# Performance work log

Hardware: AMD Instinct MI355X
Metric: run time of the kernel (lower is better)

## Reference

```python
import jax, jax.numpy as jnp
import numpy as np

N_NODES = 50000
N_EDGES = 800000
IN_FEATS = 96
HIDDEN = 48


def setup_inputs() -> dict:
    key = jax.random.key(0)
    ks = jax.random.split(key, 16)
    x = jax.random.normal(ks[0], (N_NODES, IN_FEATS), dtype=jnp.float32)
    edge_index = jax.random.randint(ks[1], (2, N_EDGES), 0, N_NODES, dtype=jnp.int32)

    def lin(k, fan_in, fan_out):
        s = 1.0 / np.sqrt(fan_in)
        return jax.random.uniform(k, (fan_in, fan_out), jnp.float32, -s, s)

    return {
        "x": x,
        "edge_index": edge_index,
        # SAGEConv layer 0: in -> hidden
        "w_self0": lin(ks[2], IN_FEATS, HIDDEN),
        "w_neigh0": lin(ks[3], IN_FEATS, HIDDEN),
        "b0": jnp.zeros((HIDDEN,), jnp.float32),
        # SAGEConv layer 1: hidden -> hidden
        "w_self1": lin(ks[4], HIDDEN, HIDDEN),
        "w_neigh1": lin(ks[5], HIDDEN, HIDDEN),
        "b1": jnp.zeros((HIDDEN,), jnp.float32),
        # SAGEConv layer 2: hidden -> hidden
        "w_self2": lin(ks[6], HIDDEN, HIDDEN),
        "w_neigh2": lin(ks[7], HIDDEN, HIDDEN),
        "b2": jnp.zeros((HIDDEN,), jnp.float32),
        # prediction head: hidden -> 1
        "w_pred": lin(ks[8], HIDDEN, 1),
        "b_pred": jnp.zeros((1,), jnp.float32),
    }


def _sage_mean(x, src, dst, deg_inv, w_self, w_neigh, b):
    # mean over in-neighbors: gather src features, segment-sum at dst, / in-degree
    agg = jax.ops.segment_sum(x[src], dst, num_segments=N_NODES) * deg_inv  # [N, F]
    return x @ w_self + agg @ w_neigh + b


def reference(x, edge_index, w_self0, w_neigh0, b0, w_self1, w_neigh1, b1,
              w_self2, w_neigh2, b2, w_pred, b_pred):
    src, dst = edge_index[0], edge_index[1]
    deg = jax.ops.segment_sum(jnp.ones((src.shape[0],), x.dtype), dst,
                              num_segments=N_NODES)
    deg_inv = (1.0 / jnp.maximum(deg, 1.0))[:, None]  # isolated nodes -> 0 agg

    h = jax.nn.relu(_sage_mean(x, src, dst, deg_inv, w_self0, w_neigh0, b0))
    h = jax.nn.relu(_sage_mean(h, src, dst, deg_inv, w_self1, w_neigh1, b1))
    h = jax.nn.relu(_sage_mean(h, src, dst, deg_inv, w_self2, w_neigh2, b2))
    return h @ w_pred + b_pred  # [N, 1]
```

## Files before the change

kernel.cpp:

```cpp
#include <hip/hip_runtime.h>
#include <hip/hip_fp16.h>


constexpr int HID = 48;
constexpr int MAXDEG = 64;
constexpr int GNB = 64;

__device__ __forceinline__ unsigned pack_h2(float a, float b) {
    __half2 h = __floats2half2_rn(a, b);
    return *reinterpret_cast<unsigned*>(&h);
}
__device__ __forceinline__ void acc_u2(float* g, uint2 u) {
    __half2 h0 = *reinterpret_cast<__half2*>(&u.x);
    __half2 h1 = *reinterpret_cast<__half2*>(&u.y);
    float2 f0 = __half22float2(h0), f1 = __half22float2(h1);
    g[0] += f0.x; g[1] += f0.y; g[2] += f1.x; g[3] += f1.y;
}
__device__ __forceinline__ void unpack_u2(float* v, uint2 u) {
    __half2 h0 = *reinterpret_cast<__half2*>(&u.x);
    __half2 h1 = *reinterpret_cast<__half2*>(&u.y);
    float2 f0 = __half22float2(h0), f1 = __half22float2(h1);
    v[0] = f0.x; v[1] = f0.y; v[2] = f1.x; v[3] = f1.y;
}
__device__ __forceinline__ void fma12_h(const uint2* __restrict__ wrow, float s,
                                        float* acc) {
    uint2 w0 = wrow[0], w1 = wrow[1], w2 = wrow[2];
    float v[12];
    unpack_u2(v + 0, w0); unpack_u2(v + 4, w1); unpack_u2(v + 8, w2);
#pragma unroll
    for (int j = 0; j < 12; ++j) acc[j] = fmaf(s, v[j], acc[j]);
}

__device__ __forceinline__ void gather_h8(const __half* __restrict__ p,
                                          const unsigned short* __restrict__ bkt,
                                          uint4 pv0, uint4 pv1, int deg, int e,
                                          int jb, int zrow, float* g) {
    float ga[12], gb[12];
#pragma unroll
    for (int j = 0; j < 12; ++j) { ga[j] = 0.0f; gb[j] = 0.0f; }
    const int sh = 16 * e;
    int idx[8];
    {
        unsigned w[8] = {pv0.x, pv0.y, pv0.z, pv0.w, pv1.x, pv1.y, pv1.z, pv1.w};
#pragma unroll
        for (int r = 0; r < 8; ++r) {
            int k = 2 * r + e;
            idx[r] = (k < deg) ? (int)((w[r] >> sh) & 0xffffu) : zrow;
        }
    }
    {
        const uint2* r0 = reinterpret_cast<const uint2*>(p + (size_t)idx[0] * HID + jb);
        const uint2* r1 = reinterpret_cast<const uint2*>(p + (size_t)idx[1] * HID + jb);
        const uint2* r2 = reinterpret_cast<const uint2*>(p + (size_t)idx[2] * HID + jb);
        const uint2* r3 = reinterpret_cast<const uint2*>(p + (size_t)idx[3] * HID + jb);
        uint2 a0 = r0[0], a1 = r0[1], a2 = r0[2];
        uint2 b0 = r1[0], b1 = r1[1], b2 = r1[2];
        uint2 c0 = r2[0], c1 = r2[1], c2 = r2[2];
        uint2 d0 = r3[0], d1 = r3[1], d2 = r3[2];
        acc_u2(ga + 0, a0); acc_u2(ga + 4, a1); acc_u2(ga + 8, a2);
        acc_u2(gb + 0, b0); acc_u2(gb + 4, b1); acc_u2(gb + 8, b2);
        acc_u2(ga + 0, c0); acc_u2(ga + 4, c1); acc_u2(ga + 8, c2);
        acc_u2(gb + 0, d0); acc_u2(gb + 4, d1); acc_u2(gb + 8, d2);
    }
    {
        const uint2* r0 = reinterpret_cast<const uint2*>(p + (size_t)idx[4] * HID + jb);
        const uint2* r1 = reinterpret_cast<const uint2*>(p + (size_t)idx[5] * HID + jb);
        const uint2* r2 = reinterpret_cast<const uint2*>(p + (size_t)idx[6] * HID + jb);
        const uint2* r3 = reinterpret_cast<const uint2*>(p + (size_t)idx[7] * HID + jb);
        uint2 a0 = r0[0], a1 = r0[1], a2 = r0[2];
        uint2 b0 = r1[0], b1 = r1[1], b2 = r1[2];
        uint2 c0 = r2[0], c1 = r2[1], c2 = r2[2];
        uint2 d0 = r3[0], d1 = r3[1], d2 = r3[2];
        acc_u2(ga + 0, a0); acc_u2(ga + 4, a1); acc_u2(ga + 8, a2);
        acc_u2(gb + 0, b0); acc_u2(gb + 4, b1); acc_u2(gb + 8, b2);
        acc_u2(ga + 0, c0); acc_u2(ga + 4, c1); acc_u2(ga + 8, c2);
        acc_u2(gb + 0, d0); acc_u2(gb + 4, d1); acc_u2(gb + 8, d2);
    }
    int i = 16 + e;
    for (; i + 6 < deg; i += 8) {
        int s0 = bkt[i], s1 = bkt[i + 2], s2 = bkt[i + 4], s3 = bkt[i + 6];
        const uint2* r0 = reinterpret_cast<const uint2*>(p + (size_t)s0 * HID + jb);
        const uint2* r1 = reinterpret_cast<const uint2*>(p + (size_t)s1 * HID + jb);
        const uint2* r2 = reinterpret_cast<const uint2*>(p + (size_t)s2 * HID + jb);
        const uint2* r3 = reinterpret_cast<const uint2*>(p + (size_t)s3 * HID + jb);
        uint2 a0 = r0[0], a1 = r0[1], a2 = r0[2];
        uint2 b0 = r1[0], b1 = r1[1], b2 = r1[2];
        uint2 c0 = r2[0], c1 = r2[1], c2 = r2[2];
        uint2 d0 = r3[0], d1 = r3[1], d2 = r3[2];
        acc_u2(ga + 0, a0); acc_u2(ga + 4, a1); acc_u2(ga + 8, a2);
        acc_u2(gb + 0, b0); acc_u2(gb + 4, b1); acc_u2(gb + 8, b2);
        acc_u2(ga + 0, c0); acc_u2(ga + 4, c1); acc_u2(ga + 8, c2);
        acc_u2(gb + 0, d0); acc_u2(gb + 4, d1); acc_u2(gb + 8, d2);
    }
    for (; i + 2 < deg; i += 4) {
        int s0 = bkt[i], s1 = bkt[i + 2];
        const uint2* r0 = reinterpret_cast<const uint2*>(p + (size_t)s0 * HID + jb);
        const uint2* r1 = reinterpret_cast<const uint2*>(p + (size_t)s1 * HID + jb);
        uint2 a0 = r0[0], a1 = r0[1], a2 = r0[2];
        uint2 b0 = r1[0], b1 = r1[1], b2 = r1[2];
        acc_u2(ga + 0, a0); acc_u2(ga + 4, a1); acc_u2(ga + 8, a2);
        acc_u2(gb + 0, b0); acc_u2(gb + 4, b1); acc_u2(gb + 8, b2);
    }
    if (i < deg) {
        const uint2* r0 = reinterpret_cast<const uint2*>(p + (size_t)bkt[i] * HID + jb);
        uint2 a0 = r0[0], a1 = r0[1], a2 = r0[2];
        acc_u2(ga + 0, a0); acc_u2(ga + 4, a1); acc_u2(ga + 8, a2);
    }
#pragma unroll
    for (int j = 0; j < 12; ++j) g[j] = ga[j] + gb[j];
#pragma unroll
    for (int j = 0; j < 12; ++j) g[j] += __shfl_xor(g[j], 4, 64);
}

__global__ __launch_bounds__(128) void fill_proj_k(
    const float* __restrict__ X, const float* __restrict__ Wn,
    const float* __restrict__ Ws, const float* __restrict__ bias,
    __half* __restrict__ p_out, float* __restrict__ s_out, int n_nodes,
    const int* __restrict__ src, const int* __restrict__ dst,
    int* __restrict__ cnt, unsigned short* __restrict__ buckets,
    int n_edges, int gemm_blocks, int cstride) {
    __shared__ float wlds[96 * HID];
    __shared__ float bias_lds[HID];
    const int t = threadIdx.x;

    if ((int)blockIdx.x >= gemm_blocks) {
        int base = (blockIdx.x - gemm_blocks) * 512 + t;
#pragma unroll
        for (int u = 0; u < 4; ++u) {
            int eidx = base + u * 128;
            if (eidx < n_edges) {
                int d = dst[eidx];
                int s = src[eidx];
                int pos = atomicAdd(&cnt[(size_t)d * cstride], 1);
                if (pos < MAXDEG) buckets[(size_t)d * MAXDEG + pos] = (unsigned short)s;
            }
        }
        return;
    }

    if (blockIdx.x == 0 && t < 24)
        reinterpret_cast<unsigned*>(p_out + (size_t)n_nodes * HID)[t] = 0u;

    const int q = t & 3;
    const int m = t >> 2;
    const int jb = q * 12;
    const int n0 = blockIdx.x * GNB + 2 * m;
    const int n1 = n0 + 1;
    const bool v0 = n0 < n_nodes, v1 = n1 < n_nodes;
    const int cn0 = v0 ? n0 : 0, cn1 = v1 ? n1 : 0;
    const float4* xr0 = reinterpret_cast<const float4*>(X + (size_t)cn0 * 96);
    const float4* xr1 = reinterpret_cast<const float4*>(X + (size_t)cn1 * 96);

    for (int i = t; i < 96 * HID; i += 128) wlds[i] = Wn[i];
    __syncthreads();
    {
        float pa[12], pb[12];
#pragma unroll
        for (int j = 0; j < 12; ++j) { pa[j] = 0.0f; pb[j] = 0.0f; }
#pragma unroll 4
        for (int k4 = 0; k4 < 24; ++k4) {
            float4 xa = xr0[k4];
            float4 xb = xr1[k4];
#pragma unroll
            for (int c = 0; c < 4; ++c) {
                float x0 = (c == 0) ? xa.x : (c == 1) ? xa.y : (c == 2) ? xa.z : xa.w;
                float x1 = (c == 0) ? xb.x : (c == 1) ? xb.y : (c == 2) ? xb.z : xb.w;
                const float4* wr =
                    reinterpret_cast<const float4*>(&wlds[(k4 * 4 + c) * HID + jb]);
#pragma unroll
                for (int j4 = 0; j4 < 3; ++j4) {
                    float4 wv = wr[j4];
                    pa[j4 * 4 + 0] = fmaf(x0, wv.x, pa[j4 * 4 + 0]);
                    pa[j4 * 4 + 1] = fmaf(x0, wv.y, pa[j4 * 4 + 1]);
                    pa[j4 * 4 + 2] = fmaf(x0, wv.z, pa[j4 * 4 + 2]);
                    pa[j4 * 4 + 3] = fmaf(x0, wv.w, pa[j4 * 4 + 3]);
                    pb[j4 * 4 + 0] = fmaf(x1, wv.x, pb[j4 * 4 + 0]);
                    pb[j4 * 4 + 1] = fmaf(x1, wv.y, pb[j4 * 4 + 1]);
                    pb[j4 * 4 + 2] = fmaf(x1, wv.z, pb[j4 * 4 + 2]);
                    pb[j4 * 4 + 3] = fmaf(x1, wv.w, pb[j4 * 4 + 3]);
                }
            }
        }
        if (v0) {
            uint2* po = reinterpret_cast<uint2*>(p_out + (size_t)n0 * HID + jb);
            po[0] = make_uint2(pack_h2(pa[0], pa[1]), pack_h2(pa[2], pa[3]));
            po[1] = make_uint2(pack_h2(pa[4], pa[5]), pack_h2(pa[6], pa[7]));
            po[2] = make_uint2(pack_h2(pa[8], pa[9]), pack_h2(pa[10], pa[11]));
        }
        if (v1) {
            uint2* po = reinterpret_cast<uint2*>(p_out + (size_t)n1 * HID + jb);
            po[0] = make_uint2(pack_h2(pb[0], pb[1]), pack_h2(pb[2], pb[3]));
            po[1] = make_uint2(pack_h2(pb[4], pb[5]), pack_h2(pb[6], pb[7]));
            po[2] = make_uint2(pack_h2(pb[8], pb[9]), pack_h2(pb[10], pb[11]));
        }
    }
    __syncthreads();

    for (int i = t; i < 96 * HID; i += 128) wlds[i] = Ws[i];
    if (t < HID) bias_lds[t] = bias[t];
    __syncthreads();
    {
        float sa[12], sb[12];
#pragma unroll
        for (int j = 0; j < 12; ++j) {
            float b = bias_lds[jb + j];
            sa[j] = b; sb[j] = b;
        }
#pragma unroll 4
        for (int k4 = 0; k4 < 24; ++k4) {
            float4 xa = xr0[k4];
            float4 xb = xr1[k4];
#pragma unroll
            for (int c = 0; c < 4; ++c) {
                float x0 = (c == 0) ? xa.x : (c == 1) ? xa.y : (c == 2) ? xa.z : xa.w;
                float x1 = (c == 0) ? xb.x : (c == 1) ? xb.y : (c == 2) ? xb.z : xb.w;
                const float4* wr =
                    reinterpret_cast<const float4*>(&wlds[(k4 * 4 + c) * HID + jb]);
#pragma unroll
                for (int j4 = 0; j4 < 3; ++j4) {
                    float4 wv = wr[j4];
                    sa[j4 * 4 + 0] = fmaf(x0, wv.x, sa[j4 * 4 + 0]);
                    sa[j4 * 4 + 1] = fmaf(x0, wv.y, sa[j4 * 4 + 1]);
                    sa[j4 * 4 + 2] = fmaf(x0, wv.z, sa[j4 * 4 + 2]);
                    sa[j4 * 4 + 3] = fmaf(x0, wv.w, sa[j4 * 4 + 3]);
                    sb[j4 * 4 + 0] = fmaf(x1, wv.x, sb[j4 * 4 + 0]);
                    sb[j4 * 4 + 1] = fmaf(x1, wv.y, sb[j4 * 4 + 1]);
                    sb[j4 * 4 + 2] = fmaf(x1, wv.z, sb[j4 * 4 + 2]);
                    sb[j4 * 4 + 3] = fmaf(x1, wv.w, sb[j4 * 4 + 3]);
                }
            }
        }
        float4* so0 = reinterpret_cast<float4*>(s_out + (size_t)cn0 * HID + jb);
        float4* so1 = reinterpret_cast<float4*>(s_out + (size_t)cn1 * HID + jb);
#pragma unroll
        for (int j4 = 0; j4 < 3; ++j4) {
            if (v0) so0[j4] = make_float4(sa[j4 * 4 + 0], sa[j4 * 4 + 1],
                                          sa[j4 * 4 + 2], sa[j4 * 4 + 3]);
            if (v1) so1[j4] = make_float4(sb[j4 * 4 + 0], sb[j4 * 4 + 1],
                                          sb[j4 * 4 + 2], sb[j4 * 4 + 3]);
        }
    }
}

__global__ __launch_bounds__(128, 6) void act_k(
    const __half* __restrict__ p_in, const float* __restrict__ s_in,
    const int* __restrict__ cnt, const unsigned short* __restrict__ buckets,
    __half* __restrict__ h_out, int n_nodes, int cstride) {
    const int t = threadIdx.x;
    if (blockIdx.x == 0 && t < 24)
        reinterpret_cast<unsigned*>(h_out + (size_t)n_nodes * HID)[t] = 0u;
    const int q = t & 3;
    const int e = (t >> 2) & 1;
    const int m = t >> 3;
    const int n = blockIdx.x * 16 + m;
    if (n >= n_nodes) return;
    const int jb = q * 12;

    const int deg_raw = cnt[(size_t)n * cstride];
    const unsigned short* bkt = buckets + (size_t)n * MAXDEG;
    const uint4 pv0 = reinterpret_cast<const uint4*>(bkt)[0];
    const uint4 pv1 = reinterpret_cast<const uint4*>(bkt)[1];
    float4 sv0, sv1, sv2;
    if (e == 0) {
        const float4* sr = reinterpret_cast<const float4*>(s_in + (size_t)n * HID + jb);
        sv0 = sr[0]; sv1 = sr[1]; sv2 = sr[2];
    }

    const int deg = min(deg_raw, MAXDEG);
    const float di = 1.0f / fmaxf((float)deg, 1.0f);
    float g[12];
    gather_h8(p_in, bkt, pv0, pv1, deg, e, jb, n_nodes, g);

    if (e == 0) {
        float h[12];
        h[0] = fmaxf(fmaf(di, g[0], sv0.x), 0.0f);
        h[1] = fmaxf(fmaf(di, g[1], sv0.y), 0.0f);
        h[2] = fmaxf(fmaf(di, g[2], sv0.z), 0.0f);
        h[3] = fmaxf(fmaf(di, g[3], sv0.w), 0.0f);
        h[4] = fmaxf(fmaf(di, g[4], sv1.x), 0.0f);
        h[5] = fmaxf(fmaf(di, g[5], sv1.y), 0.0f);
        h[6] = fmaxf(fmaf(di, g[6], sv1.z), 0.0f);
        h[7] = fmaxf(fmaf(di, g[7], sv1.w), 0.0f);
        h[8] = fmaxf(fmaf(di, g[8], sv2.x), 0.0f);
        h[9] = fmaxf(fmaf(di, g[9], sv2.y), 0.0f);
        h[10] = fmaxf(fmaf(di, g[10], sv2.z), 0.0f);
        h[11] = fmaxf(fmaf(di, g[11], sv2.w), 0.0f);
        uint2* ho = reinterpret_cast<uint2*>(h_out + (size_t)n * HID + jb);
        ho[0] = make_uint2(pack_h2(h[0], h[1]), pack_h2(h[2], h[3]));
        ho[1] = make_uint2(pack_h2(h[4], h[5]), pack_h2(h[6], h[7]));
        ho[2] = make_uint2(pack_h2(h[8], h[9]), pack_h2(h[10], h[11]));
    }
}

template <bool LAST>
__global__ __launch_bounds__(128, 6) void layer_k(
    const __half* __restrict__ h_in, const int* __restrict__ cnt,
    const unsigned short* __restrict__ buckets, const float* __restrict__ wn,
    const float* __restrict__ ws, const float* __restrict__ bn,
    const float* __restrict__ w_pred, const float* __restrict__ b_pred,
    __half* __restrict__ h_out, float* __restrict__ out, int n_nodes,
    int cstride) {
    __shared__ uint2 wn_s[HID * HID / 4];
    __shared__ uint2 ws_s[HID * HID / 4];
    __shared__ float bn_lds[HID];
    __shared__ float wp_lds[HID];

    const int t = threadIdx.x;
    const int q = t & 3;
    const int e = (t >> 2) & 1;
    const int m = t >> 3;
    const int n = blockIdx.x * 16 + m;
    const bool nv = n < n_nodes;
    const int cn = nv ? n : 0;
    const int jb = q * 12;

    if (!LAST && blockIdx.x == 0 && t < 24)
        reinterpret_cast<unsigned*>(h_out + (size_t)n_nodes * HID)[t] = 0u;

    const int deg_raw = cnt[(size_t)cn * cstride];
    const unsigned short* bkt = buckets + (size_t)cn * MAXDEG;
    const uint4 pv0 = reinterpret_cast<const uint4*>(bkt)[0];
    const uint4 pv1 = reinterpret_cast<const uint4*>(bkt)[1];
    const uint2* hr = reinterpret_cast<const uint2*>(h_in + (size_t)cn * HID + jb);
    uint2 ha = hr[0], hb = hr[1], hc = hr[2];

    for (int i4 = t; i4 < HID * HID / 4; i4 += 128) {
        float4 a = reinterpret_cast<const float4*>(wn)[i4];
        float4 b = reinterpret_cast<const float4*>(ws)[i4];
        wn_s[i4] = make_uint2(pack_h2(a.x, a.y), pack_h2(a.z, a.w));
        ws_s[i4] = make_uint2(pack_h2(b.x, b.y), pack_h2(b.z, b.w));
    }
    if (t < HID) bn_lds[t] = bn[t];
    if (LAST && t < HID) wp_lds[t] = w_pred[t];
    __syncthreads();

    if (!nv) return;

    const int deg = min(deg_raw, MAXDEG);
    const float di = 1.0f / fmaxf((float)deg, 1.0f);
    float g[12];
    gather_h8(h_in, bkt, pv0, pv1, deg, e, jb, n_nodes, g);
#pragma unroll
    for (int j = 0; j < 12; ++j) g[j] *= di;

    float hs_own[12];
    unpack_u2(hs_own + 0, ha); unpack_u2(hs_own + 4, hb); unpack_u2(hs_own + 8, hc);

    float acc[12];
#pragma unroll
    for (int j = 0; j < 12; ++j) acc[j] = (e == 0) ? bn_lds[jb + j] : 0.0f;

    const int kb = e * 24;
#pragma unroll
    for (int kk = 0; kk < 24; ++kk) {
        const int k = kb + kk;
        const int srcl = (t & ~3) | (k / 12);
        float gs = __shfl(g[kk % 12], srcl, 64);
        float hv = __shfl(hs_own[kk % 12], srcl, 64);
        fma12_h(&wn_s[(k * HID + jb) >> 2], gs, acc);
        fma12_h(&ws_s[(k * HID + jb) >> 2], hv, acc);
    }
#pragma unroll
    for (int j = 0; j < 12; ++j) acc[j] += __shfl_xor(acc[j], 4, 64);

    if (LAST) {
        float s = 0.0f;
#pragma unroll
        for (int j = 0; j < 12; ++j) s = fmaf(fmaxf(acc[j], 0.0f), wp_lds[jb + j], s);
        s += __shfl_xor(s, 1, 64);
        s += __shfl_xor(s, 2, 64);
        if ((t & 7) == 0) out[n] = s + b_pred[0];
        return;
    }

    if (e == 0) {
        float h[12];
#pragma unroll
        for (int j = 0; j < 12; ++j) h[j] = fmaxf(acc[j], 0.0f);
        uint2* ho = reinterpret_cast<uint2*>(h_out + (size_t)n * HID + jb);
        ho[0] = make_uint2(pack_h2(h[0], h[1]), pack_h2(h[2], h[3]));
        ho[1] = make_uint2(pack_h2(h[4], h[5]), pack_h2(h[6], h[7]));
        ho[2] = make_uint2(pack_h2(h[8], h[9]), pack_h2(h[10], h[11]));
    }
}

extern "C" void kernel_launch(void* const* d_in, const int* in_sizes, int n_in,
                              void* d_out, int out_size, void* d_ws, size_t ws_size,
                              hipStream_t stream) {
    const float* x        = (const float*)d_in[0];
    const int*   ei       = (const int*)d_in[1];
    const float* w_self0  = (const float*)d_in[2];
    const float* w_neigh0 = (const float*)d_in[3];
    const float* b0       = (const float*)d_in[4];
    const float* w_self1  = (const float*)d_in[5];
    const float* w_neigh1 = (const float*)d_in[6];
    const float* b1       = (const float*)d_in[7];
    const float* w_self2  = (const float*)d_in[8];
    const float* w_neigh2 = (const float*)d_in[9];
    const float* b2       = (const float*)d_in[10];
    const float* w_pred   = (const float*)d_in[11];
    const float* b_pred   = (const float*)d_in[12];

    const int n_nodes = in_sizes[0] / 96;
    const int n_edges = in_sizes[1] / 2;
    const int* src = ei;
    const int* dst = ei + n_edges;

    const size_t need_fixed = (size_t)n_nodes * MAXDEG * 2
                            + 3 * ((size_t)(n_nodes + 1) * HID * 2)
                            + (size_t)n_nodes * HID * 4;
    int cstride = (need_fixed + (size_t)n_nodes * 4 * 4 <= ws_size) ? 4 : 1;

    char* wsb = (char*)d_ws;
    int* cnt                = (int*)wsb;              wsb += (size_t)n_nodes * cstride * 4;
    unsigned short* buckets = (unsigned short*)wsb;   wsb += (size_t)n_nodes * MAXDEG * 2;
    __half* p0 = (__half*)wsb;                        wsb += (size_t)(n_nodes + 1) * HID * 2;
    __half* h1 = (__half*)wsb;                        wsb += (size_t)(n_nodes + 1) * HID * 2;
    __half* h2 = (__half*)wsb;                        wsb += (size_t)(n_nodes + 1) * HID * 2;
    float* s0 = (float*)wsb;                          wsb += (size_t)n_nodes * HID * 4;
    float* out = (float*)d_out;

    const int gnb = (n_nodes + GNB - 1) / GNB;
    const int fb = (n_edges + 511) / 512;
    const int lb = (n_nodes + 15) / 16;

    hipMemsetAsync(cnt, 0, (size_t)n_nodes * cstride * 4, stream);

    fill_proj_k<<<gnb + fb, 128, 0, stream>>>(x, w_neigh0, w_self0, b0, p0, s0,
                                              n_nodes, src, dst, cnt, buckets,
                                              n_edges, gnb, cstride);
    act_k<<<lb, 128, 0, stream>>>(p0, s0, cnt, buckets, h1, n_nodes, cstride);
    layer_k<false><<<lb, 128, 0, stream>>>(h1, cnt, buckets, w_neigh1, w_self1,
                                           b1, nullptr, nullptr, h2, nullptr,
                                           n_nodes, cstride);
    layer_k<true><<<lb, 128, 0, stream>>>(h2, cnt, buckets, w_neigh2, w_self2,
                                          b2, w_pred, b_pred, nullptr, out,
                                          n_nodes, cstride);
}
```

Baseline: 216.6 us.

## Move layer-0 self projection into aggregation kernel and pad feature rows to 64

The self-term projection x@W_self0+b0 moves out of the fill/projection kernel and into act_k, which recomputes it from x while doing the neighbor gather. This removes the fp32 s0 intermediate write and read. Feature rows are padded to a 64-half stride so each row sits on one 128-byte line, and the gather is templated to prefetch 4 or 2 index vectors up front. In exchange act_k holds an 18KB weight tile in LDS and its occupancy hint drops to 4, and it rereads x.

```diff
diff --git a/kernel.cpp b/kernel.cpp
--- a/kernel.cpp
+++ b/kernel.cpp
@@ -4,6 +4,7 @@
 
 constexpr int HID = 48;
 constexpr int MAXDEG = 64;
+constexpr int RSTRIDE = 64;
 constexpr int GNB = 64;
 
 __device__ __forceinline__ unsigned pack_h2(float a, float b) {
@@ -31,28 +32,26 @@
     for (int j = 0; j < 12; ++j) acc[j] = fmaf(s, v[j], acc[j]);
 }
 
-__device__ __forceinline__ void gather_h8(const __half* __restrict__ p,
-                                          const unsigned short* __restrict__ bkt,
-                                          uint4 pv0, uint4 pv1, int deg, int e,
-                                          int jb, int zrow, float* g) {
+template <int NB>
+__device__ __forceinline__ void gather_pad(const __half* __restrict__ p,
+                                           const unsigned short* __restrict__ bkt,
+                                           const uint4 (&pw)[NB], int deg, int e,
+                                           int jb, int zrow, float* g) {
     float ga[12], gb[12];
 #pragma unroll
     for (int j = 0; j < 12; ++j) { ga[j] = 0.0f; gb[j] = 0.0f; }
     const int sh = 16 * e;
-    int idx[8];
-    {
-        unsigned w[8] = {pv0.x, pv0.y, pv0.z, pv0.w, pv1.x, pv1.y, pv1.z, pv1.w};
-#pragma unroll
-        for (int r = 0; r < 8; ++r) {
-            int k = 2 * r + e;
-            idx[r] = (k < deg) ? (int)((w[r] >> sh) & 0xffffu) : zrow;
-        }
-    }
-    {
-        const uint2* r0 = reinterpret_cast<const uint2*>(p + (size_t)idx[0] * HID + jb);
-        const uint2* r1 = reinterpret_cast<const uint2*>(p + (size_t)idx[1] * HID + jb);
-        const uint2* r2 = reinterpret_cast<const uint2*>(p + (size_t)idx[2] * HID + jb);
-        const uint2* r3 = reinterpret_cast<const uint2*>(p + (size_t)idx[3] * HID + jb);
+#pragma unroll
+    for (int b = 0; b < NB; ++b) {
+        const int k0 = 8 * b + e;
+        int i0 = (k0 < deg)     ? (int)((pw[b].x >> sh) & 0xffffu) : zrow;
+        int i1 = (k0 + 2 < deg) ? (int)((pw[b].y >> sh) & 0xffffu) : zrow;
+        int i2 = (k0 + 4 < deg) ? (int)((pw[b].z >> sh) & 0xffffu) : zrow;
+        int i3 = (k0 + 6 < deg) ? (int)((pw[b].w >> sh) & 0xffffu) : zrow;
+        const uint2* r0 = reinterpret_cast<const uint2*>(p + (size_t)i0 * RSTRIDE + jb);
+        const uint2* r1 = reinterpret_cast<const uint2*>(p + (size_t)i1 * RSTRIDE + jb);
+        const uint2* r2 = reinterpret_cast<const uint2*>(p + (size_t)i2 * RSTRIDE + jb);
+        const uint2* r3 = reinterpret_cast<const uint2*>(p + (size_t)i3 * RSTRIDE + jb);
         uint2 a0 = r0[0], a1 = r0[1], a2 = r0[2];
         uint2 b0 = r1[0], b1 = r1[1], b2 = r1[2];
         uint2 c0 = r2[0], c1 = r2[1], c2 = r2[2];
@@ -62,11 +61,13 @@
         acc_u2(ga + 0, c0); acc_u2(ga + 4, c1); acc_u2(ga + 8, c2);
         acc_u2(gb + 0, d0); acc_u2(gb + 4, d1); acc_u2(gb + 8, d2);
     }
-    {
-        const uint2* r0 = reinterpret_cast<const uint2*>(p + (size_t)idx[4] * HID + jb);
-        const uint2* r1 = reinterpret_cast<const uint2*>(p + (size_t)idx[5] * HID + jb);
-        const uint2* r2 = reinterpret_cast<const uint2*>(p + (size_t)idx[6] * HID + jb);
-        const uint2* r3 = reinterpret_cast<const uint2*>(p + (size_t)idx[7] * HID + jb);
+    int i = 8 * NB + e;
+    for (; i + 6 < deg; i += 8) {
+        int s0 = bkt[i], s1 = bkt[i + 2], s2 = bkt[i + 4], s3 = bkt[i + 6];
+        const uint2* r0 = reinterpret_cast<const uint2*>(p + (size_t)s0 * RSTRIDE + jb);
+        const uint2* r1 = reinterpret_cast<const uint2*>(p + (size_t)s1 * RSTRIDE + jb);
+        const uint2* r2 = reinterpret_cast<const uint2*>(p + (size_t)s2 * RSTRIDE + jb);
+        const uint2* r3 = reinterpret_cast<const uint2*>(p + (size_t)s3 * RSTRIDE + jb);
         uint2 a0 = r0[0], a1 = r0[1], a2 = r0[2];
         uint2 b0 = r1[0], b1 = r1[1], b2 = r1[2];
         uint2 c0 = r2[0], c1 = r2[1], c2 = r2[2];
@@ -76,33 +77,17 @@
         acc_u2(ga + 0, c0); acc_u2(ga + 4, c1); acc_u2(ga + 8, c2);
         acc_u2(gb + 0, d0); acc_u2(gb + 4, d1); acc_u2(gb + 8, d2);
     }
-    int i = 16 + e;
-    for (; i + 6 < deg; i += 8) {
-        int s0 = bkt[i], s1 = bkt[i + 2], s2 = bkt[i + 4], s3 = bkt[i + 6];
-        const uint2* r0 = reinterpret_cast<const uint2*>(p + (size_t)s0 * HID + jb);
-        const uint2* r1 = reinterpret_cast<const uint2*>(p + (size_t)s1 * HID + jb);
-        const uint2* r2 = reinterpret_cast<const uint2*>(p + (size_t)s2 * HID + jb);
-        const uint2* r3 = reinterpret_cast<const uint2*>(p + (size_t)s3 * HID + jb);
-        uint2 a0 = r0[0], a1 = r0[1], a2 = r0[2];
-        uint2 b0 = r1[0], b1 = r1[1], b2 = r1[2];
-        uint2 c0 = r2[0], c1 = r2[1], c2 = r2[2];
-        uint2 d0 = r3[0], d1 = r3[1], d2 = r3[2];
-        acc_u2(ga + 0, a0); acc_u2(ga + 4, a1); acc_u2(ga + 8, a2);
-        acc_u2(gb + 0, b0); acc_u2(gb + 4, b1); acc_u2(gb + 8, b2);
-        acc_u2(ga + 0, c0); acc_u2(ga + 4, c1); acc_u2(ga + 8, c2);
-        acc_u2(gb + 0, d0); acc_u2(gb + 4, d1); acc_u2(gb + 8, d2);
-    }
     for (; i + 2 < deg; i += 4) {
         int s0 = bkt[i], s1 = bkt[i + 2];
-        const uint2* r0 = reinterpret_cast<const uint2*>(p + (size_t)s0 * HID + jb);
-        const uint2* r1 = reinterpret_cast<const uint2*>(p + (size_t)s1 * HID + jb);
+        const uint2* r0 = reinterpret_cast<const uint2*>(p + (size_t)s0 * RSTRIDE + jb);
+        const uint2* r1 = reinterpret_cast<const uint2*>(p + (size_t)s1 * RSTRIDE + jb);
         uint2 a0 = r0[0], a1 = r0[1], a2 = r0[2];
         uint2 b0 = r1[0], b1 = r1[1], b2 = r1[2];
         acc_u2(ga + 0, a0); acc_u2(ga + 4, a1); acc_u2(ga + 8, a2);
         acc_u2(gb + 0, b0); acc_u2(gb + 4, b1); acc_u2(gb + 8, b2);
     }
     if (i < deg) {
-        const uint2* r0 = reinterpret_cast<const uint2*>(p + (size_t)bkt[i] * HID + jb);
+        const uint2* r0 = reinterpret_cast<const uint2*>(p + (size_t)bkt[i] * RSTRIDE + jb);
         uint2 a0 = r0[0], a1 = r0[1], a2 = r0[2];
         acc_u2(ga + 0, a0); acc_u2(ga + 4, a1); acc_u2(ga + 8, a2);
     }
@@ -114,13 +99,11 @@
 
 __global__ __launch_bounds__(128) void fill_proj_k(
     const float* __restrict__ X, const float* __restrict__ Wn,
-    const float* __restrict__ Ws, const float* __restrict__ bias,
-    __half* __restrict__ p_out, float* __restrict__ s_out, int n_nodes,
+    __half* __restrict__ p_out, int n_nodes,
     const int* __restrict__ src, const int* __restrict__ dst,
     int* __restrict__ cnt, unsigned short* __restrict__ buckets,
     int n_edges, int gemm_blocks, int cstride) {
     __shared__ float wlds[96 * HID];
-    __shared__ float bias_lds[HID];
     const int t = threadIdx.x;
 
     if ((int)blockIdx.x >= gemm_blocks) {
@@ -138,8 +121,8 @@
         return;
     }
 
-    if (blockIdx.x == 0 && t < 24)
-        reinterpret_cast<unsigned*>(p_out + (size_t)n_nodes * HID)[t] = 0u;
+    if (blockIdx.x == 0 && t < 32)
+        reinterpret_cast<unsigned*>(p_out + (size_t)n_nodes * RSTRIDE)[t] = 0u;
 
     const int q = t & 3;
     const int m = t >> 2;
@@ -153,139 +136,117 @@
 
     for (int i = t; i < 96 * HID; i += 128) wlds[i] = Wn[i];
     __syncthreads();
-    {
-        float pa[12], pb[12];
-#pragma unroll
-        for (int j = 0; j < 12; ++j) { pa[j] = 0.0f; pb[j] = 0.0f; }
+
+    float pa[12], pb[12];
+#pragma unroll
+    for (int j = 0; j < 12; ++j) { pa[j] = 0.0f; pb[j] = 0.0f; }
 #pragma unroll 4
-        for (int k4 = 0; k4 < 24; ++k4) {
-            float4 xa = xr0[k4];
-            float4 xb = xr1[k4];
-#pragma unroll
-            for (int c = 0; c < 4; ++c) {
-                float x0 = (c == 0) ? xa.x : (c == 1) ? xa.y : (c == 2) ? xa.z : xa.w;
-                float x1 = (c == 0) ? xb.x : (c == 1) ? xb.y : (c == 2) ? xb.z : xb.w;
-                const float4* wr =
-                    reinterpret_cast<const float4*>(&wlds[(k4 * 4 + c) * HID + jb]);
-#pragma unroll
-                for (int j4 = 0; j4 < 3; ++j4) {
-                    float4 wv = wr[j4];
-                    pa[j4 * 4 + 0] = fmaf(x0, wv.x, pa[j4 * 4 + 0]);
-                    pa[j4 * 4 + 1] = fmaf(x0, wv.y, pa[j4 * 4 + 1]);
-                    pa[j4 * 4 + 2] = fmaf(x0, wv.z, pa[j4 * 4 + 2]);
-                    pa[j4 * 4 + 3] = fmaf(x0, wv.w, pa[j4 * 4 + 3]);
-                    pb[j4 * 4 + 0] = fmaf(x1, wv.x, pb[j4 * 4 + 0]);
-                    pb[j4 * 4 + 1] = fmaf(x1, wv.y, pb[j4 * 4 + 1]);
-                    pb[j4 * 4 + 2] = fmaf(x1, wv.z, pb[j4 * 4 + 2]);
-                    pb[j4 * 4 + 3] = fmaf(x1, wv.w, pb[j4 * 4 + 3]);
-                }
+    for (int k4 = 0; k4 < 24; ++k4) {
+        float4 xa = xr0[k4];
+        float4 xb = xr1[k4];
+#pragma unroll
+        for (int c = 0; c < 4; ++c) {
+            float x0 = (c == 0) ? xa.x : (c == 1) ? xa.y : (c == 2) ? xa.z : xa.w;
+            float x1 = (c == 0) ? xb.x : (c == 1) ? xb.y : (c == 2) ? xb.z : xb.w;
+            const float4* wr =
+                reinterpret_cast<const float4*>(&wlds[(k4 * 4 + c) * HID + jb]);
+#pragma unroll
+            for (int j4 = 0; j4 < 3; ++j4) {
+                float4 wv = wr[j4];
+                pa[j4 * 4 + 0] = fmaf(x0, wv.x, pa[j4 * 4 + 0]);
+                pa[j4 * 4 + 1] = fmaf(x0, wv.y, pa[j4 * 4 + 1]);
+                pa[j4 * 4 + 2] = fmaf(x0, wv.z, pa[j4 * 4 + 2]);
+                pa[j4 * 4 + 3] = fmaf(x0, wv.w, pa[j4 * 4 + 3]);
+                pb[j4 * 4 + 0] = fmaf(x1, wv.x, pb[j4 * 4 + 0]);
+                pb[j4 * 4 + 1] = fmaf(x1, wv.y, pb[j4 * 4 + 1]);
+                pb[j4 * 4 + 2] = fmaf(x1, wv.z, pb[j4 * 4 + 2]);
+                pb[j4 * 4 + 3] = fmaf(x1, wv.w, pb[j4 * 4 + 3]);
             }
         }
-        if (v0) {
-            uint2* po = reinterpret_cast<uint2*>(p_out + (size_t)n0 * HID + jb);
-            po[0] = make_uint2(pack_h2(pa[0], pa[1]), pack_h2(pa[2], pa[3]));
-            po[1] = make_uint2(pack_h2(pa[4], pa[5]), pack_h2(pa[6], pa[7]));
-            po[2] = make_uint2(pack_h2(pa[8], pa[9]), pack_h2(pa[10], pa[11]));
-        }
-        if (v1) {
-            uint2* po = reinterpret_cast<uint2*>(p_out + (size_t)n1 * HID + jb);
-            po[0] = make_uint2(pack_h2(pb[0], pb[1]), pack_h2(pb[2], pb[3]));
-            po[1] = make_uint2(pack_h2(pb[4], pb[5]), pack_h2(pb[6], pb[7]));
-            po[2] = make_uint2(pack_h2(pb[8], pb[9]), pack_h2(pb[10], pb[11]));
-        }
-    }
-    __syncthreads();
-
-    for (int i = t; i < 96 * HID; i += 128) wlds[i] = Ws[i];
-    if (t < HID) bias_lds[t] = bias[t];
-    __syncthreads();
-    {
-        float sa[12], sb[12];
-#pragma unroll
-        for (int j = 0; j < 12; ++j) {
-            float b = bias_lds[jb + j];
-            sa[j] = b; sb[j] = b;
-        }
-#pragma unroll 4
-        for (int k4 = 0; k4 < 24; ++k4) {
-            float4 xa = xr0[k4];
-            float4 xb = xr1[k4];
-#pragma unroll
-            for (int c = 0; c < 4; ++c) {
-                float x0 = (c == 0) ? xa.x : (c == 1) ? xa.y : (c == 2) ? xa.z : xa.w;
-                float x1 = (c == 0) ? xb.x : (c == 1) ? xb.y : (c == 2) ? xb.z : xb.w;
-                const float4* wr =
-                    reinterpret_cast<const float4*>(&wlds[(k4 * 4 + c) * HID + jb]);
-#pragma unroll
-                for (int j4 = 0; j4 < 3; ++j4) {
-                    float4 wv = wr[j4];
-                    sa[j4 * 4 + 0] = fmaf(x0, wv.x, sa[j4 * 4 + 0]);
-                    sa[j4 * 4 + 1] = fmaf(x0, wv.y, sa[j4 * 4 + 1]);
-                    sa[j4 * 4 + 2] = fmaf(x0, wv.z, sa[j4 * 4 + 2]);
-                    sa[j4 * 4 + 3] = fmaf(x0, wv.w, sa[j4 * 4 + 3]);
-                    sb[j4 * 4 + 0] = fmaf(x1, wv.x, sb[j4 * 4 + 0]);
-                    sb[j4 * 4 + 1] = fmaf(x1, wv.y, sb[j4 * 4 + 1]);
-                    sb[j4 * 4 + 2] = fmaf(x1, wv.z, sb[j4 * 4 + 2]);
-                    sb[j4 * 4 + 3] = fmaf(x1, wv.w, sb[j4 * 4 + 3]);
-                }
-            }
-        }
-        float4* so0 = reinterpret_cast<float4*>(s_out + (size_t)cn0 * HID + jb);
-        float4* so1 = reinterpret_cast<float4*>(s_out + (size_t)cn1 * HID + jb);
-#pragma unroll
-        for (int j4 = 0; j4 < 3; ++j4) {
-            if (v0) so0[j4] = make_float4(sa[j4 * 4 + 0], sa[j4 * 4 + 1],
-                                          sa[j4 * 4 + 2], sa[j4 * 4 + 3]);
-            if (v1) so1[j4] = make_float4(sb[j4 * 4 + 0], sb[j4 * 4 + 1],
-                                          sb[j4 * 4 + 2], sb[j4 * 4 + 3]);
-        }
-    }
-}
-
-__global__ __launch_bounds__(128, 6) void act_k(
-    const __half* __restrict__ p_in, const float* __restrict__ s_in,
+    }
+    if (v0) {
+        uint2* po = reinterpret_cast<uint2*>(p_out + (size_t)n0 * RSTRIDE + jb);
+        po[0] = make_uint2(pack_h2(pa[0], pa[1]), pack_h2(pa[2], pa[3]));
+        po[1] = make_uint2(pack_h2(pa[4], pa[5]), pack_h2(pa[6], pa[7]));
+        po[2] = make_uint2(pack_h2(pa[8], pa[9]), pack_h2(pa[10], pa[11]));
+    }
+    if (v1) {
+        uint2* po = reinterpret_cast<uint2*>(p_out + (size_t)n1 * RSTRIDE + jb);
+        po[0] = make_uint2(pack_h2(pb[0], pb[1]), pack_h2(pb[2], pb[3]));
+        po[1] = make_uint2(pack_h2(pb[4], pb[5]), pack_h2(pb[6], pb[7]));
+        po[2] = make_uint2(pack_h2(pb[8], pb[9]), pack_h2(pb[10], pb[11]));
+    }
+}
+
+__global__ __launch_bounds__(128, 4) void act_k(
+    const __half* __restrict__ p_in, const float* __restrict__ X,
+    const float* __restrict__ ws, const float* __restrict__ bias,
     const int* __restrict__ cnt, const unsigned short* __restrict__ buckets,
     __half* __restrict__ h_out, int n_nodes, int cstride) {
+    __shared__ float wlds[96 * HID];
+    __shared__ float b_lds[HID];
+
     const int t = threadIdx.x;
-    if (blockIdx.x == 0 && t < 24)
-        reinterpret_cast<unsigned*>(h_out + (size_t)n_nodes * HID)[t] = 0u;
+    if (blockIdx.x == 0 && t < 32)
+        reinterpret_cast<unsigned*>(h_out + (size_t)n_nodes * RSTRIDE)[t] = 0u;
+
     const int q = t & 3;
     const int e = (t >> 2) & 1;
     const int m = t >> 3;
     const int n = blockIdx.x * 16 + m;
-    if (n >= n_nodes) return;
+    const bool nv = n < n_nodes;
+    const int cn = nv ? n : 0;
     const int jb = q * 12;
 
-    const int deg_raw = cnt[(size_t)n * cstride];
-    const unsigned short* bkt = buckets + (size_t)n * MAXDEG;
-    const uint4 pv0 = reinterpret_cast<const uint4*>(bkt)[0];
-    const uint4 pv1 = reinterpret_cast<const uint4*>(bkt)[1];
-    float4 sv0, sv1, sv2;
-    if (e == 0) {
-        const float4* sr = reinterpret_cast<const float4*>(s_in + (size_t)n * HID + jb);
-        sv0 = sr[0]; sv1 = sr[1]; sv2 = sr[2];
-    }
+    const int deg_raw = cnt[(size_t)cn * cstride];
+    const unsigned short* bkt = buckets + (size_t)cn * MAXDEG;
+    uint4 pw[4];
+#pragma unroll
+    for (int b = 0; b < 4; ++b) pw[b] = reinterpret_cast<const uint4*>(bkt)[b];
+
+    for (int i4 = t; i4 < 96 * HID / 4; i4 += 128)
+        reinterpret_cast<float4*>(wlds)[i4] = reinterpret_cast<const float4*>(ws)[i4];
+    if (t < HID) b_lds[t] = bias[t];
+    __syncthreads();
+
+    if (!nv) return;
 
     const int deg = min(deg_raw, MAXDEG);
     const float di = 1.0f / fmaxf((float)deg, 1.0f);
+
     float g[12];
-    gather_h8(p_in, bkt, pv0, pv1, deg, e, jb, n_nodes, g);
+    gather_pad<4>(p_in, bkt, pw, deg, e, jb, n_nodes, g);
+
+    float s[12];
+#pragma unroll
+    for (int j = 0; j < 12; ++j) s[j] = (e == 0) ? b_lds[jb + j] : 0.0f;
+    const float4* xr = reinterpret_cast<const float4*>(X + (size_t)cn * 96 + 48 * e);
+#pragma unroll 4
+    for (int k4 = 0; k4 < 12; ++k4) {
+        float4 xv = xr[k4];
+#pragma unroll
+        for (int c = 0; c < 4; ++c) {
+            float xc = (c == 0) ? xv.x : (c == 1) ? xv.y : (c == 2) ? xv.z : xv.w;
+            const float4* wr = reinterpret_cast<const float4*>(
+                &wlds[(48 * e + k4 * 4 + c) * HID + jb]);
+#pragma unroll
+            for (int j4 = 0; j4 < 3; ++j4) {
+                float4 wv = wr[j4];
+                s[j4 * 4 + 0] = fmaf(xc, wv.x, s[j4 * 4 + 0]);
+                s[j4 * 4 + 1] = fmaf(xc, wv.y, s[j4 * 4 + 1]);
+                s[j4 * 4 + 2] = fmaf(xc, wv.z, s[j4 * 4 + 2]);
+                s[j4 * 4 + 3] = fmaf(xc, wv.w, s[j4 * 4 + 3]);
+            }
+        }
+    }
+#pragma unroll
+    for (int j = 0; j < 12; ++j) s[j] += __shfl_xor(s[j], 4, 64);
 
     if (e == 0) {
         float h[12];
-        h[0] = fmaxf(fmaf(di, g[0], sv0.x), 0.0f);
-        h[1] = fmaxf(fmaf(di, g[1], sv0.y), 0.0f);
-        h[2] = fmaxf(fmaf(di, g[2], sv0.z), 0.0f);
-        h[3] = fmaxf(fmaf(di, g[3], sv0.w), 0.0f);
-        h[4] = fmaxf(fmaf(di, g[4], sv1.x), 0.0f);
-        h[5] = fmaxf(fmaf(di, g[5], sv1.y), 0.0f);
-        h[6] = fmaxf(fmaf(di, g[6], sv1.z), 0.0f);
-        h[7] = fmaxf(fmaf(di, g[7], sv1.w), 0.0f);
-        h[8] = fmaxf(fmaf(di, g[8], sv2.x), 0.0f);
-        h[9] = fmaxf(fmaf(di, g[9], sv2.y), 0.0f);
-        h[10] = fmaxf(fmaf(di, g[10], sv2.z), 0.0f);
-        h[11] = fmaxf(fmaf(di, g[11], sv2.w), 0.0f);
-        uint2* ho = reinterpret_cast<uint2*>(h_out + (size_t)n * HID + jb);
+#pragma unroll
+        for (int j = 0; j < 12; ++j) h[j] = fmaxf(fmaf(di, g[j], s[j]), 0.0f);
+        uint2* ho = reinterpret_cast<uint2*>(h_out + (size_t)n * RSTRIDE + jb);
         ho[0] = make_uint2(pack_h2(h[0], h[1]), pack_h2(h[2], h[3]));
         ho[1] = make_uint2(pack_h2(h[4], h[5]), pack_h2(h[6], h[7]));
         ho[2] = make_uint2(pack_h2(h[8], h[9]), pack_h2(h[10], h[11]));
@@ -314,14 +275,15 @@
     const int cn = nv ? n : 0;
     const int jb = q * 12;
 
-    if (!LAST && blockIdx.x == 0 && t < 24)
-        reinterpret_cast<unsigned*>(h_out + (size_t)n_nodes * HID)[t] = 0u;
+    if (!LAST && blockIdx.x == 0 && t < 32)
+        reinterpret_cast<unsigned*>(h_out + (size_t)n_nodes * RSTRIDE)[t] = 0u;
 
     const int deg_raw = cnt[(size_t)cn * cstride];
     const unsigned short* bkt = buckets + (size_t)cn * MAXDEG;
-    const uint4 pv0 = reinterpret_cast<const uint4*>(bkt)[0];
-    const uint4 pv1 = reinterpret_cast<const uint4*>(bkt)[1];
-    const uint2* hr = reinterpret_cast<const uint2*>(h_in + (size_t)cn * HID + jb);
+    uint4 pw[2];
+#pragma unroll
+    for (int b = 0; b < 2; ++b) pw[b] = reinterpret_cast<const uint4*>(bkt)[b];
+    const uint2* hr = reinterpret_cast<const uint2*>(h_in + (size_t)cn * RSTRIDE + jb);
     uint2 ha = hr[0], hb = hr[1], hc = hr[2];
 
     for (int i4 = t; i4 < HID * HID / 4; i4 += 128) {
@@ -339,7 +301,7 @@
     const int deg = min(deg_raw, MAXDEG);
     const float di = 1.0f / fmaxf((float)deg, 1.0f);
     float g[12];
-    gather_h8(h_in, bkt, pv0, pv1, deg, e, jb, n_nodes, g);
+    gather_pad<2>(h_in, bkt, pw, deg, e, jb, n_nodes, g);
 #pragma unroll
     for (int j = 0; j < 12; ++j) g[j] *= di;
 
@@ -377,7 +339,7 @@
         float h[12];
 #pragma unroll
         for (int j = 0; j < 12; ++j) h[j] = fmaxf(acc[j], 0.0f);
-        uint2* ho = reinterpret_cast<uint2*>(h_out + (size_t)n * HID + jb);
+        uint2* ho = reinterpret_cast<uint2*>(h_out + (size_t)n * RSTRIDE + jb);
         ho[0] = make_uint2(pack_h2(h[0], h[1]), pack_h2(h[2], h[3]));
         ho[1] = make_uint2(pack_h2(h[4], h[5]), pack_h2(h[6], h[7]));
         ho[2] = make_uint2(pack_h2(h[8], h[9]), pack_h2(h[10], h[11]));
@@ -407,17 +369,15 @@
     const int* dst = ei + n_edges;
 
     const size_t need_fixed = (size_t)n_nodes * MAXDEG * 2
-                            + 3 * ((size_t)(n_nodes + 1) * HID * 2)
-                            + (size_t)n_nodes * HID * 4;
+                            + 3 * ((size_t)(n_nodes + 1) * RSTRIDE * 2);
     int cstride = (need_fixed + (size_t)n_nodes * 4 * 4 <= ws_size) ? 4 : 1;
 
     char* wsb = (char*)d_ws;
     int* cnt                = (int*)wsb;              wsb += (size_t)n_nodes * cstride * 4;
     unsigned short* buckets = (unsigned short*)wsb;   wsb += (size_t)n_nodes * MAXDEG * 2;
-    __half* p0 = (__half*)wsb;                        wsb += (size_t)(n_nodes + 1) * HID * 2;
-    __half* h1 = (__half*)wsb;                        wsb += (size_t)(n_nodes + 1) * HID * 2;
-    __half* h2 = (__half*)wsb;                        wsb += (size_t)(n_nodes + 1) * HID * 2;
-    float* s0 = (float*)wsb;                          wsb += (size_t)n_nodes * HID * 4;
+    __half* p0 = (__half*)wsb;                        wsb += (size_t)(n_nodes + 1) * RSTRIDE * 2;
+    __half* h1 = (__half*)wsb;                        wsb += (size_t)(n_nodes + 1) * RSTRIDE * 2;
+    __half* h2 = (__half*)wsb;                        wsb += (size_t)(n_nodes + 1) * RSTRIDE * 2;
     float* out = (float*)d_out;
 
     const int gnb = (n_nodes + GNB - 1) / GNB;
@@ -426,10 +386,10 @@
 
     hipMemsetAsync(cnt, 0, (size_t)n_nodes * cstride * 4, stream);
 
-    fill_proj_k<<<gnb + fb, 128, 0, stream>>>(x, w_neigh0, w_self0, b0, p0, s0,
-                                              n_nodes, src, dst, cnt, buckets,
-                                              n_edges, gnb, cstride);
-    act_k<<<lb, 128, 0, stream>>>(p0, s0, cnt, buckets, h1, n_nodes, cstride);
+    fill_proj_k<<<gnb + fb, 128, 0, stream>>>(x, w_neigh0, p0, n_nodes, src, dst,
+                                              cnt, buckets, n_edges, gnb, cstride);
+    act_k<<<lb, 128, 0, stream>>>(p0, x, w_self0, b0, cnt, buckets, h1,
+                                  n_nodes, cstride);
     layer_k<false><<<lb, 128, 0, stream>>>(h1, cnt, buckets, w_neigh1, w_self1,
                                            b1, nullptr, nullptr, h2, nullptr,
                                            n_nodes, cstride);
```

After: 215.4 us. No clear change (-0.6%).
